# Optimization experiments

Hardware: AMD Instinct MI355X
Metric: run time of the kernel (lower is better)

## Reference

```python
import jax, jax.numpy as jnp
import numpy as np

NUM_HEADS = 16
HEAD_DIM = 64
INPUT_DIM = 1024
EMBED_DIM = NUM_HEADS * HEAD_DIM  # 1024


def setup_inputs() -> dict:
    key = jax.random.key(0)
    ks = jax.random.split(key, 9)
    B, S = 4, 2048
    scale = 1.0 / np.sqrt(INPUT_DIM)
    return {
        "q": jax.random.normal(ks[0], (B, S, INPUT_DIM), dtype=jnp.float32),
        "k": jax.random.normal(ks[1], (B, S, INPUT_DIM), dtype=jnp.float32),
        "v": jax.random.normal(ks[2], (B, S, INPUT_DIM), dtype=jnp.float32),
        "Wq": jax.random.normal(ks[3], (INPUT_DIM, EMBED_DIM), dtype=jnp.float32) * scale,
        "bq": jax.random.normal(ks[4], (EMBED_DIM,), dtype=jnp.float32) * 0.02,
        "Wk": jax.random.normal(ks[5], (INPUT_DIM, EMBED_DIM), dtype=jnp.float32) * scale,
        "bk": jax.random.normal(ks[6], (EMBED_DIM,), dtype=jnp.float32) * 0.02,
        "Wv": jax.random.normal(ks[7], (INPUT_DIM, EMBED_DIM), dtype=jnp.float32) * scale,
        "bv": jax.random.normal(ks[8], (EMBED_DIM,), dtype=jnp.float32) * 0.02,
    }


def reference(q, k, v, Wq, bq, Wk, bk, Wv, bv):
    B, Sq, _ = q.shape
    Sk = k.shape[1]
    # QKV projections (dropout_prob=0 -> identity; ReLU on value path)
    query = (q @ Wq + bq).reshape(B, Sq, NUM_HEADS, HEAD_DIM).transpose(0, 2, 1, 3)  # [B,H,Sq,D]
    key_ = (k @ Wk + bk).reshape(B, Sk, NUM_HEADS, HEAD_DIM).transpose(0, 2, 1, 3)   # [B,H,Sk,D]
    value = jax.nn.relu(v @ Wv + bv).reshape(B, Sk, NUM_HEADS, HEAD_DIM).transpose(0, 2, 1, 3)
    scores = jnp.einsum("bhqd,bhkd->bhqk", query, key_) / np.sqrt(HEAD_DIM).astype(np.float32)
    p_attn = jax.nn.softmax(scores, axis=-1)
    x = jnp.einsum("bhqk,bhkd->bhqd", p_attn, value)  # [B,H,Sq,D]
    return x.transpose(0, 2, 1, 3).reshape(B, Sq, EMBED_DIM)
```

## Files before the change

kernel.cpp:

```cpp
#include <hip/hip_runtime.h>
#include <hip/hip_bf16.h>
#include <stdint.h>

#define BB    4
#define NH    16
#define SEQ   2048
#define DH    64
#define EMB   1024
#define KD    1024
#define MROWS 8192

typedef short  short8  __attribute__((ext_vector_type(8)));
typedef float  f32x4   __attribute__((ext_vector_type(4)));
typedef float  f32x16  __attribute__((ext_vector_type(16)));

typedef const __attribute__((address_space(1))) void* gas_t;
typedef __attribute__((address_space(3))) void*       las_t;
#define GLD16(g, l) __builtin_amdgcn_global_load_lds((gas_t)(g), (las_t)(l), 16, 0, 0)

__device__ __forceinline__ unsigned short f2bf(float f) {
    unsigned u = __float_as_uint(f);
    u += 0x7fffu + ((u >> 16) & 1u);
    return (unsigned short)(u >> 16);
}
__device__ __forceinline__ unsigned packbf(float lo, float hi) {
    union { __hip_bfloat162 h; unsigned u; } cv;
    cv.h = __float22bfloat162_rn(make_float2(lo, hi));
    return cv.u;
}

__global__ __launch_bounds__(256) void conv3_kernel(const float* __restrict__ qf,
                                                    const float* __restrict__ kf,
                                                    const float* __restrict__ vf,
                                                    unsigned short* __restrict__ dst) {
    const int p = blockIdx.z;
    const float* src = (p == 0) ? qf : (p == 1) ? kf : vf;
    unsigned short* d = dst + (size_t)p * ((size_t)MROWS * KD);
    const size_t i = ((size_t)blockIdx.x * 256 + threadIdx.x) * 8;
    float4 f0 = *(const float4*)(src + i);
    float4 f1 = *(const float4*)(src + i + 4);
    uint4 u;
    u.x = packbf(f0.x, f0.y); u.y = packbf(f0.z, f0.w);
    u.z = packbf(f1.x, f1.y); u.w = packbf(f1.z, f1.w);
    *(uint4*)(d + i) = u;
}

__global__ __launch_bounds__(256) void wt_kernel(const float* __restrict__ Wq,
                                                 const float* __restrict__ Wk,
                                                 const float* __restrict__ Wv,
                                                 unsigned short* __restrict__ Wt) {
    __shared__ float tsh[64 * 68];
    const int p = blockIdx.z;
    const float* W = (p == 0) ? Wq : (p == 1) ? Wk : Wv;
    unsigned short* dst = Wt + (size_t)p * (KD * EMB);
    const int k0 = blockIdx.x * 64, n0 = blockIdx.y * 64;
    const int t = threadIdx.x;
    {
        const int r = t >> 2, c4 = (t & 3) * 16;
        const float* g = W + (size_t)(k0 + r) * EMB + n0 + c4;
        float* row = &tsh[r * 68 + c4];
        *(float4*)(row + 0)  = *(const float4*)(g + 0);
        *(float4*)(row + 4)  = *(const float4*)(g + 4);
        *(float4*)(row + 8)  = *(const float4*)(g + 8);
        *(float4*)(row + 12) = *(const float4*)(g + 12);
    }
    __syncthreads();
    {
        const int j = t >> 2, kp = (t & 3) * 16;
        unsigned ub[8];
#pragma unroll
        for (int ii = 0; ii < 8; ++ii)
            ub[ii] = packbf(tsh[(kp + 2 * ii) * 68 + j], tsh[(kp + 2 * ii + 1) * 68 + j]);
        unsigned short* o = dst + (size_t)(n0 + j) * KD + k0 + kp;
        *(uint4*)(o + 0) = uint4{ub[0], ub[1], ub[2], ub[3]};
        *(uint4*)(o + 8) = uint4{ub[4], ub[5], ub[6], ub[7]};
    }
}

__global__ __launch_bounds__(256) void proj_kernel(
    const unsigned short* __restrict__ AbfBase, const unsigned short* __restrict__ WtBase,
    const float* __restrict__ bq, const float* __restrict__ bk, const float* __restrict__ bv,
    unsigned short* __restrict__ Qg, unsigned short* __restrict__ Kg,
    unsigned short* __restrict__ Vt)
{
    __shared__ __align__(16) unsigned short smem[17408];
    unsigned short* Ash = smem;
    unsigned short* Bsh = smem + 8192;

    const int p = blockIdx.z;
    const unsigned short* Abf = AbfBase + (size_t)p * ((size_t)MROWS * KD);
    const unsigned short* Wp  = WtBase  + (size_t)p * (KD * EMB);
    const float* bias = (p == 0) ? bq : (p == 1) ? bk : bv;
    unsigned short* dst = (p == 0) ? Qg : (p == 1) ? Kg : Vt;

    const int row0 = blockIdx.x * 128;
    const int col0 = blockIdx.y * 128;
    const int t = threadIdx.x, lane = t & 63, wv = t >> 6;
    const int ln15 = lane & 15, q4 = lane >> 4;
    const int wm = wv & 1, wn = wv >> 1;

    f32x4 acc[4][4];
#pragma unroll
    for (int i = 0; i < 4; ++i)
#pragma unroll
        for (int j = 0; j < 4; ++j)
#pragma unroll
            for (int r = 0; r < 4; ++r) acc[i][j][r] = 0.f;

    const int lr = lane >> 3, lc = (lane & 7) ^ lr;
    const unsigned short* gA = Abf + (size_t)(row0 + wv * 32 + lr) * KD + lc * 8;
    const unsigned short* gB = Wp  + (size_t)(col0 + wv * 32 + lr) * KD + lc * 8;
    unsigned short* lA = Ash + wv * 32 * 64;
    unsigned short* lB = Bsh + wv * 32 * 64;

    for (int k0 = 0; k0 < KD; k0 += 64) {
#pragma unroll
        for (int i = 0; i < 4; ++i) {
            GLD16(gA + (size_t)i * 8 * KD + k0, lA + i * 512);
            GLD16(gB + (size_t)i * 8 * KD + k0, lB + i * 512);
        }
        __syncthreads();
#pragma unroll
        for (int kk = 0; kk < 2; ++kk) {
            short8 af[4], bfr[4];
#pragma unroll
            for (int mi = 0; mi < 4; ++mi) {
                const int r = wm * 64 + mi * 16 + ln15;
                af[mi] = *(const short8*)&Ash[r * 64 + (((kk << 2) | q4) ^ (r & 7)) * 8];
            }
#pragma unroll
            for (int ni = 0; ni < 4; ++ni) {
                const int r = wn * 64 + ni * 16 + ln15;
                bfr[ni] = *(const short8*)&Bsh[r * 64 + (((kk << 2) | q4) ^ (r & 7)) * 8];
            }
#pragma unroll
            for (int mi = 0; mi < 4; ++mi)
#pragma unroll
                for (int ni = 0; ni < 4; ++ni)
                    acc[mi][ni] = __builtin_amdgcn_mfma_f32_16x16x32_bf16(
                        af[mi], bfr[ni], acc[mi][ni], 0, 0, 0);
        }
        __syncthreads();
    }

    float bvv[4];
#pragma unroll
    for (int ni = 0; ni < 4; ++ni) bvv[ni] = bias[col0 + wn * 64 + ni * 16 + ln15];
    const float scq = 0.18033688011112042f;

    unsigned short* Tsh = smem;
#pragma unroll
    for (int mi = 0; mi < 4; ++mi)
#pragma unroll
        for (int ni = 0; ni < 4; ++ni)
#pragma unroll
            for (int r = 0; r < 4; ++r) {
                const int mr = wm * 64 + mi * 16 + q4 * 4 + r;
                const int ec = wn * 64 + ni * 16 + ln15;
                float vv = acc[mi][ni][r] + bvv[ni];
                if (p == 0) vv *= scq;
                if (p == 2) vv = vv > 0.f ? vv : 0.f;
                Tsh[mr * 136 + ec] = f2bf(vv);
            }
    __syncthreads();

    if (p < 2) {
        const int mr = t >> 1, hsel = t & 1;
        const int m = row0 + mr, bi = m >> 11, s = m & 2047;
        const int hh = (col0 >> 6) + hsel;
        const unsigned short* src = &Tsh[mr * 136 + hsel * 64];
        unsigned short* o = dst + ((size_t)(bi * NH + hh) * SEQ + s) * DH;
#pragma unroll
        for (int c = 0; c < 8; ++c)
            *(uint4*)(o + 8 * c) = *(const uint4*)(src + 8 * c);
    } else {
        const int e = t >> 1, sh2 = t & 1;
        const int n = col0 + e, hh = n >> 6, dd = n & 63;
        const int bi = row0 >> 11, sbase = (row0 & 2047) + sh2 * 64;
        unsigned ub[32];
#pragma unroll
        for (int i = 0; i < 32; ++i)
            ub[i] = (unsigned)Tsh[(sh2 * 64 + 2 * i) * 136 + e] |
                    ((unsigned)Tsh[(sh2 * 64 + 2 * i + 1) * 136 + e] << 16);
        unsigned short* o = dst + ((size_t)(bi * NH + hh) * DH + dd) * SEQ + sbase;
#pragma unroll
        for (int c = 0; c < 8; ++c)
            *(uint4*)(o + 8 * c) = uint4{ub[4 * c], ub[4 * c + 1], ub[4 * c + 2], ub[4 * c + 3]};
    }
}

__global__ __launch_bounds__(256) void attn_kernel(
    const unsigned short* __restrict__ Qg, const unsigned short* __restrict__ Kg,
    const unsigned short* __restrict__ Vt, float* __restrict__ out)
{
    __shared__ __align__(16) unsigned char smem[34816];
    unsigned short* Ksh = (unsigned short*)smem;
    unsigned short* Vsh = (unsigned short*)smem + 64 * 72;
    float* Osh = (float*)smem;

    const int qb = blockIdx.x, hh = blockIdx.y, bb = blockIdx.z;
    const int t = threadIdx.x, lane = t & 63, wv = t >> 6;
    const int ln31 = lane & 31, h2 = lane >> 5;
    const size_t bh = (size_t)(bb * NH + hh);
    const unsigned short* Qp = Qg + bh * (SEQ * DH);
    const unsigned short* Kp = Kg + bh * (SEQ * DH);
    const unsigned short* Vp = Vt + bh * (DH * SEQ);
    const int q0 = qb * 128 + wv * 32;

    short8 qf[4];
#pragma unroll
    for (int dc = 0; dc < 4; ++dc)
        qf[dc] = *(const short8*)(Qp + (size_t)(q0 + ln31) * DH + h2 * 8 + dc * 16);

    short8 ones;
#pragma unroll
    for (int i = 0; i < 8; ++i) ones[i] = (short)0x3F80;

    f32x16 accO[2], accL;
#pragma unroll
    for (int i = 0; i < 16; ++i) { accO[0][i] = 0.f; accO[1][i] = 0.f; accL[i] = 0.f; }

    const int srow = t >> 2, sp = (t & 3) * 16;
    const unsigned short* gk = Kp + (size_t)srow * DH + sp;
    const unsigned short* gv = Vp + (size_t)srow * SEQ + sp;
    unsigned short* lk = &Ksh[srow * 72 + sp];
    unsigned short* lv = &Vsh[srow * 72 + sp];

    for (int kt0 = 0; kt0 < SEQ; kt0 += 64) {
        __syncthreads();
        *(short8*)lk       = *(const short8*)(gk + (size_t)kt0 * DH);
        *(short8*)(lk + 8) = *(const short8*)(gk + (size_t)kt0 * DH + 8);
        *(short8*)lv       = *(const short8*)(gv + kt0);
        *(short8*)(lv + 8) = *(const short8*)(gv + kt0 + 8);
        __syncthreads();

        f32x16 st[2];
#pragma unroll
        for (int kt = 0; kt < 2; ++kt) {
#pragma unroll
            for (int i = 0; i < 16; ++i) st[kt][i] = 0.f;
#pragma unroll
            for (int dc = 0; dc < 4; ++dc) {
                short8 kf = *(const short8*)&Ksh[(kt * 32 + ln31) * 72 + h2 * 8 + dc * 16];
                st[kt] = __builtin_amdgcn_mfma_f32_32x32x16_bf16(kf, qf[dc], st[kt], 0, 0, 0);
            }
        }
#pragma unroll
        for (int kt = 0; kt < 2; ++kt)
#pragma unroll
            for (int r = 0; r < 16; ++r)
                st[kt][r] = __builtin_amdgcn_exp2f(st[kt][r]);

#pragma unroll
        for (int kt = 0; kt < 2; ++kt) {
            unsigned ow[8], xw[8];
#pragma unroll
            for (int i = 0; i < 8; ++i) {
                ow[i] = packbf(st[kt][2 * i], st[kt][2 * i + 1]);
                xw[i] = (unsigned)__shfl_xor((int)ow[i], 32);
            }
#pragma unroll
            for (int kc = 0; kc < 2; ++kc) {
                union { unsigned u[4]; short8 v; } pf;
                pf.u[0] = h2 ? xw[4 * kc + 2] : ow[4 * kc + 0];
                pf.u[1] = h2 ? xw[4 * kc + 3] : ow[4 * kc + 1];
                pf.u[2] = h2 ? ow[4 * kc + 2] : xw[4 * kc + 0];
                pf.u[3] = h2 ? ow[4 * kc + 3] : xw[4 * kc + 1];
                const int nc = kt * 2 + kc;
                accL = __builtin_amdgcn_mfma_f32_32x32x16_bf16(ones, pf.v, accL, 0, 0, 0);
#pragma unroll
                for (int dt = 0; dt < 2; ++dt) {
                    short8 vf = *(const short8*)&Vsh[(dt * 32 + ln31) * 72 + nc * 16 + h2 * 8];
                    accO[dt] = __builtin_amdgcn_mfma_f32_32x32x16_bf16(vf, pf.v, accO[dt], 0, 0, 0);
                }
            }
        }
    }

    const float inv = 1.0f / accL[0];
    __syncthreads();
#pragma unroll
    for (int dt = 0; dt < 2; ++dt)
#pragma unroll
        for (int r = 0; r < 16; ++r) {
            const int d = dt * 32 + (r & 3) + 8 * (r >> 2) + 4 * h2;
            Osh[(wv * 32 + ln31) * 68 + d] = accO[dt][r] * inv;
        }
    __syncthreads();
    const int r128 = t >> 1, dh = t & 1;
    float* op = out + (((size_t)(bb * SEQ + qb * 128 + r128) * NH + hh) << 6) + dh * 32;
    const float* osrc = &Osh[r128 * 68 + dh * 32];
#pragma unroll
    for (int c = 0; c < 8; ++c)
        *(float4*)(op + 4 * c) = *(const float4*)(osrc + 4 * c);
}

extern "C" void kernel_launch(void* const* d_in, const int* in_sizes, int n_in,
                              void* d_out, int out_size, void* d_ws, size_t ws_size,
                              hipStream_t stream) {
    const float* qf = (const float*)d_in[0];
    const float* kf = (const float*)d_in[1];
    const float* vf = (const float*)d_in[2];
    const float* Wq = (const float*)d_in[3];
    const float* bq = (const float*)d_in[4];
    const float* Wk = (const float*)d_in[5];
    const float* bk = (const float*)d_in[6];
    const float* Wv = (const float*)d_in[7];
    const float* bv = (const float*)d_in[8];

    char* ws = (char*)d_ws;
    unsigned short* Wt  = (unsigned short*)ws;
    unsigned short* Qg  = (unsigned short*)(ws + 6291456);
    unsigned short* Kg  = Qg + 8388608;
    unsigned short* Vt  = Kg + 8388608;
    unsigned short* Ab  = Vt + 8388608;
    float* out = (float*)d_out;

    wt_kernel<<<dim3(16, 16, 3), 256, 0, stream>>>(Wq, Wk, Wv, Wt);
    conv3_kernel<<<dim3(4096, 1, 3), 256, 0, stream>>>(qf, kf, vf, Ab);
    proj_kernel<<<dim3(64, 8, 3), 256, 0, stream>>>(Ab, Wt, bq, bk, bv, Qg, Kg, Vt);
    attn_kernel<<<dim3(16, 16, 4), 256, 0, stream>>>(Qg, Kg, Vt, out);
}
```

Measured before the change: 350.9 us.

## Enlarge projection GEMM tile to 256 rows and store attention output directly

The projection GEMM now computes 256x128 tiles per block, with each wave holding an 8x4 accumulator grid. This halves the grid and cuts weight reloads per output row, at the cost of more registers, more LDS, and a two-pass epilogue through shared memory. The attention kernel drops its LDS staging of the output and writes float4 fragments straight from registers to global memory. That shrinks its shared memory and removes two barriers, but the global writes become less contiguous.

```diff
diff --git a/kernel.cpp b/kernel.cpp
--- a/kernel.cpp
+++ b/kernel.cpp
@@ -83,9 +83,9 @@
     unsigned short* __restrict__ Qg, unsigned short* __restrict__ Kg,
     unsigned short* __restrict__ Vt)
 {
-    __shared__ __align__(16) unsigned short smem[17408];
+    __shared__ __align__(16) unsigned short smem[24576];
     unsigned short* Ash = smem;
-    unsigned short* Bsh = smem + 8192;
+    unsigned short* Bsh = smem + 16384;
 
     const int p = blockIdx.z;
     const unsigned short* Abf = AbfBase + (size_t)p * ((size_t)MROWS * KD);
@@ -93,48 +93,50 @@
     const float* bias = (p == 0) ? bq : (p == 1) ? bk : bv;
     unsigned short* dst = (p == 0) ? Qg : (p == 1) ? Kg : Vt;
 
-    const int row0 = blockIdx.x * 128;
+    const int row0 = blockIdx.x * 256;
     const int col0 = blockIdx.y * 128;
     const int t = threadIdx.x, lane = t & 63, wv = t >> 6;
     const int ln15 = lane & 15, q4 = lane >> 4;
     const int wm = wv & 1, wn = wv >> 1;
 
-    f32x4 acc[4][4];
-#pragma unroll
-    for (int i = 0; i < 4; ++i)
+    f32x4 acc[8][4];
+#pragma unroll
+    for (int i = 0; i < 8; ++i)
 #pragma unroll
         for (int j = 0; j < 4; ++j)
 #pragma unroll
             for (int r = 0; r < 4; ++r) acc[i][j][r] = 0.f;
 
     const int lr = lane >> 3, lc = (lane & 7) ^ lr;
-    const unsigned short* gA = Abf + (size_t)(row0 + wv * 32 + lr) * KD + lc * 8;
+    const unsigned short* gA = Abf + (size_t)(row0 + wv * 64 + lr) * KD + lc * 8;
     const unsigned short* gB = Wp  + (size_t)(col0 + wv * 32 + lr) * KD + lc * 8;
-    unsigned short* lA = Ash + wv * 32 * 64;
+    unsigned short* lA = Ash + wv * 64 * 64;
     unsigned short* lB = Bsh + wv * 32 * 64;
 
     for (int k0 = 0; k0 < KD; k0 += 64) {
 #pragma unroll
-        for (int i = 0; i < 4; ++i) {
+        for (int i = 0; i < 8; ++i)
             GLD16(gA + (size_t)i * 8 * KD + k0, lA + i * 512);
+#pragma unroll
+        for (int i = 0; i < 4; ++i)
             GLD16(gB + (size_t)i * 8 * KD + k0, lB + i * 512);
-        }
         __syncthreads();
 #pragma unroll
         for (int kk = 0; kk < 2; ++kk) {
-            short8 af[4], bfr[4];
-#pragma unroll
-            for (int mi = 0; mi < 4; ++mi) {
-                const int r = wm * 64 + mi * 16 + ln15;
-                af[mi] = *(const short8*)&Ash[r * 64 + (((kk << 2) | q4) ^ (r & 7)) * 8];
-            }
+            const int ck = (kk << 2) | q4;
+            short8 af[8], bfr[4];
 #pragma unroll
             for (int ni = 0; ni < 4; ++ni) {
                 const int r = wn * 64 + ni * 16 + ln15;
-                bfr[ni] = *(const short8*)&Bsh[r * 64 + (((kk << 2) | q4) ^ (r & 7)) * 8];
-            }
-#pragma unroll
-            for (int mi = 0; mi < 4; ++mi)
+                bfr[ni] = *(const short8*)&Bsh[r * 64 + (ck ^ (r & 7)) * 8];
+            }
+#pragma unroll
+            for (int mi = 0; mi < 8; ++mi) {
+                const int r = wm * 128 + mi * 16 + ln15;
+                af[mi] = *(const short8*)&Ash[r * 64 + (ck ^ (r & 7)) * 8];
+            }
+#pragma unroll
+            for (int mi = 0; mi < 8; ++mi)
 #pragma unroll
                 for (int ni = 0; ni < 4; ++ni)
                     acc[mi][ni] = __builtin_amdgcn_mfma_f32_16x16x32_bf16(
@@ -150,42 +152,48 @@
 
     unsigned short* Tsh = smem;
 #pragma unroll
-    for (int mi = 0; mi < 4; ++mi)
-#pragma unroll
-        for (int ni = 0; ni < 4; ++ni)
-#pragma unroll
-            for (int r = 0; r < 4; ++r) {
-                const int mr = wm * 64 + mi * 16 + q4 * 4 + r;
-                const int ec = wn * 64 + ni * 16 + ln15;
-                float vv = acc[mi][ni][r] + bvv[ni];
-                if (p == 0) vv *= scq;
-                if (p == 2) vv = vv > 0.f ? vv : 0.f;
-                Tsh[mr * 136 + ec] = f2bf(vv);
-            }
-    __syncthreads();
-
-    if (p < 2) {
-        const int mr = t >> 1, hsel = t & 1;
-        const int m = row0 + mr, bi = m >> 11, s = m & 2047;
-        const int hh = (col0 >> 6) + hsel;
-        const unsigned short* src = &Tsh[mr * 136 + hsel * 64];
-        unsigned short* o = dst + ((size_t)(bi * NH + hh) * SEQ + s) * DH;
-#pragma unroll
-        for (int c = 0; c < 8; ++c)
-            *(uint4*)(o + 8 * c) = *(const uint4*)(src + 8 * c);
-    } else {
-        const int e = t >> 1, sh2 = t & 1;
-        const int n = col0 + e, hh = n >> 6, dd = n & 63;
-        const int bi = row0 >> 11, sbase = (row0 & 2047) + sh2 * 64;
-        unsigned ub[32];
-#pragma unroll
-        for (int i = 0; i < 32; ++i)
-            ub[i] = (unsigned)Tsh[(sh2 * 64 + 2 * i) * 136 + e] |
-                    ((unsigned)Tsh[(sh2 * 64 + 2 * i + 1) * 136 + e] << 16);
-        unsigned short* o = dst + ((size_t)(bi * NH + hh) * DH + dd) * SEQ + sbase;
-#pragma unroll
-        for (int c = 0; c < 8; ++c)
-            *(uint4*)(o + 8 * c) = uint4{ub[4 * c], ub[4 * c + 1], ub[4 * c + 2], ub[4 * c + 3]};
+    for (int h = 0; h < 2; ++h) {
+        if (wm == h) {
+#pragma unroll
+            for (int mi = 0; mi < 8; ++mi)
+#pragma unroll
+                for (int ni = 0; ni < 4; ++ni)
+#pragma unroll
+                    for (int r = 0; r < 4; ++r) {
+                        const int mr = mi * 16 + q4 * 4 + r;
+                        const int ec = wn * 64 + ni * 16 + ln15;
+                        float vv = acc[mi][ni][r] + bvv[ni];
+                        if (p == 0) vv *= scq;
+                        if (p == 2) vv = vv > 0.f ? vv : 0.f;
+                        Tsh[mr * 136 + ec] = f2bf(vv);
+                    }
+        }
+        __syncthreads();
+        if (p < 2) {
+            const int mr = t >> 1, hsel = t & 1;
+            const int m = row0 + h * 128 + mr, bi = m >> 11, s = m & 2047;
+            const int hh = (col0 >> 6) + hsel;
+            const unsigned short* src = &Tsh[mr * 136 + hsel * 64];
+            unsigned short* o = dst + ((size_t)(bi * NH + hh) * SEQ + s) * DH;
+#pragma unroll
+            for (int c = 0; c < 8; ++c)
+                *(uint4*)(o + 8 * c) = *(const uint4*)(src + 8 * c);
+        } else {
+            const int e = t >> 1, sh2 = t & 1;
+            const int n = col0 + e, hh = n >> 6, dd = n & 63;
+            const int bi = row0 >> 11;
+            const int sbase = (row0 & 2047) + h * 128 + sh2 * 64;
+            unsigned ub[32];
+#pragma unroll
+            for (int i = 0; i < 32; ++i)
+                ub[i] = (unsigned)Tsh[(sh2 * 64 + 2 * i) * 136 + e] |
+                        ((unsigned)Tsh[(sh2 * 64 + 2 * i + 1) * 136 + e] << 16);
+            unsigned short* o = dst + ((size_t)(bi * NH + hh) * DH + dd) * SEQ + sbase;
+#pragma unroll
+            for (int c = 0; c < 8; ++c)
+                *(uint4*)(o + 8 * c) = uint4{ub[4 * c], ub[4 * c + 1], ub[4 * c + 2], ub[4 * c + 3]};
+        }
+        __syncthreads();
     }
 }
 
@@ -193,10 +201,9 @@
     const unsigned short* __restrict__ Qg, const unsigned short* __restrict__ Kg,
     const unsigned short* __restrict__ Vt, float* __restrict__ out)
 {
-    __shared__ __align__(16) unsigned char smem[34816];
+    __shared__ __align__(16) unsigned char smem[18432];
     unsigned short* Ksh = (unsigned short*)smem;
     unsigned short* Vsh = (unsigned short*)smem + 64 * 72;
-    float* Osh = (float*)smem;
 
     const int qb = blockIdx.x, hh = blockIdx.y, bb = blockIdx.z;
     const int t = threadIdx.x, lane = t & 63, wv = t >> 6;
@@ -278,21 +285,18 @@
     }
 
     const float inv = 1.0f / accL[0];
-    __syncthreads();
+    float* orow = out + ((size_t)(bb * SEQ + q0 + ln31) * NH + hh) * 64;
 #pragma unroll
     for (int dt = 0; dt < 2; ++dt)
 #pragma unroll
-        for (int r = 0; r < 16; ++r) {
-            const int d = dt * 32 + (r & 3) + 8 * (r >> 2) + 4 * h2;
-            Osh[(wv * 32 + ln31) * 68 + d] = accO[dt][r] * inv;
-        }
-    __syncthreads();
-    const int r128 = t >> 1, dh = t & 1;
-    float* op = out + (((size_t)(bb * SEQ + qb * 128 + r128) * NH + hh) << 6) + dh * 32;
-    const float* osrc = &Osh[r128 * 68 + dh * 32];
-#pragma unroll
-    for (int c = 0; c < 8; ++c)
-        *(float4*)(op + 4 * c) = *(const float4*)(osrc + 4 * c);
+        for (int g = 0; g < 4; ++g) {
+            float4 w;
+            w.x = accO[dt][4 * g + 0] * inv;
+            w.y = accO[dt][4 * g + 1] * inv;
+            w.z = accO[dt][4 * g + 2] * inv;
+            w.w = accO[dt][4 * g + 3] * inv;
+            *(float4*)(orow + dt * 32 + 4 * h2 + 8 * g) = w;
+        }
 }
 
 extern "C" void kernel_launch(void* const* d_in, const int* in_sizes, int n_in,
@@ -318,6 +322,6 @@
 
     wt_kernel<<<dim3(16, 16, 3), 256, 0, stream>>>(Wq, Wk, Wv, Wt);
     conv3_kernel<<<dim3(4096, 1, 3), 256, 0, stream>>>(qf, kf, vf, Ab);
-    proj_kernel<<<dim3(64, 8, 3), 256, 0, stream>>>(Ab, Wt, bq, bk, bv, Qg, Kg, Vt);
+    proj_kernel<<<dim3(32, 8, 3), 256, 0, stream>>>(Ab, Wt, bq, bk, bv, Qg, Kg, Vt);
     attn_kernel<<<dim3(16, 16, 4), 256, 0, stream>>>(Qg, Kg, Vt, out);
 }
```

Result: slower. 386.5 us (+10.2%).

## Load K/V MFMA fragments directly from global memory, drop LDS staging

Applied to the files above, without the earlier changes.

The attention kernel no longer stages K and V tiles in shared memory with barriers. Each wave now loads its MFMA operand fragments straight from global memory into registers, and the output is written directly from accumulators without an LDS transpose. This removes the two barriers per tile and the LDS traffic. In exchange, each of the four waves re-reads the same K/V tile from global/L2, which quadruples that traffic, and the loads become less coalesced and raise register pressure.

```diff
diff --git a/kernel.cpp b/kernel.cpp
--- a/kernel.cpp
+++ b/kernel.cpp
@@ -193,18 +193,13 @@
     const unsigned short* __restrict__ Qg, const unsigned short* __restrict__ Kg,
     const unsigned short* __restrict__ Vt, float* __restrict__ out)
 {
-    __shared__ __align__(16) unsigned char smem[34816];
-    unsigned short* Ksh = (unsigned short*)smem;
-    unsigned short* Vsh = (unsigned short*)smem + 64 * 72;
-    float* Osh = (float*)smem;
-
     const int qb = blockIdx.x, hh = blockIdx.y, bb = blockIdx.z;
     const int t = threadIdx.x, lane = t & 63, wv = t >> 6;
     const int ln31 = lane & 31, h2 = lane >> 5;
     const size_t bh = (size_t)(bb * NH + hh);
     const unsigned short* Qp = Qg + bh * (SEQ * DH);
-    const unsigned short* Kp = Kg + bh * (SEQ * DH);
-    const unsigned short* Vp = Vt + bh * (DH * SEQ);
+    const unsigned short* Kp = Kg + bh * (SEQ * DH) + (size_t)ln31 * DH  + h2 * 8;
+    const unsigned short* Vp = Vt + bh * (DH * SEQ) + (size_t)ln31 * SEQ + h2 * 8;
     const int q0 = qb * 128 + wv * 32;
 
     short8 qf[4];
@@ -220,19 +215,20 @@
 #pragma unroll
     for (int i = 0; i < 16; ++i) { accO[0][i] = 0.f; accO[1][i] = 0.f; accL[i] = 0.f; }
 
-    const int srow = t >> 2, sp = (t & 3) * 16;
-    const unsigned short* gk = Kp + (size_t)srow * DH + sp;
-    const unsigned short* gv = Vp + (size_t)srow * SEQ + sp;
-    unsigned short* lk = &Ksh[srow * 72 + sp];
-    unsigned short* lv = &Vsh[srow * 72 + sp];
-
     for (int kt0 = 0; kt0 < SEQ; kt0 += 64) {
-        __syncthreads();
-        *(short8*)lk       = *(const short8*)(gk + (size_t)kt0 * DH);
-        *(short8*)(lk + 8) = *(const short8*)(gk + (size_t)kt0 * DH + 8);
-        *(short8*)lv       = *(const short8*)(gv + kt0);
-        *(short8*)(lv + 8) = *(const short8*)(gv + kt0 + 8);
-        __syncthreads();
+        short8 kfr[2][4];
+#pragma unroll
+        for (int kt = 0; kt < 2; ++kt)
+#pragma unroll
+            for (int dc = 0; dc < 4; ++dc)
+                kfr[kt][dc] = *(const short8*)(Kp + (size_t)(kt0 + kt * 32) * DH + dc * 16);
+
+        short8 vfr[2][4];
+#pragma unroll
+        for (int dt = 0; dt < 2; ++dt)
+#pragma unroll
+            for (int nc = 0; nc < 4; ++nc)
+                vfr[dt][nc] = *(const short8*)(Vp + (size_t)(dt * 32) * SEQ + kt0 + nc * 16);
 
         f32x16 st[2];
 #pragma unroll
@@ -240,10 +236,8 @@
 #pragma unroll
             for (int i = 0; i < 16; ++i) st[kt][i] = 0.f;
 #pragma unroll
-            for (int dc = 0; dc < 4; ++dc) {
-                short8 kf = *(const short8*)&Ksh[(kt * 32 + ln31) * 72 + h2 * 8 + dc * 16];
-                st[kt] = __builtin_amdgcn_mfma_f32_32x32x16_bf16(kf, qf[dc], st[kt], 0, 0, 0);
-            }
+            for (int dc = 0; dc < 4; ++dc)
+                st[kt] = __builtin_amdgcn_mfma_f32_32x32x16_bf16(kfr[kt][dc], qf[dc], st[kt], 0, 0, 0);
         }
 #pragma unroll
         for (int kt = 0; kt < 2; ++kt)
@@ -269,30 +263,25 @@
                 const int nc = kt * 2 + kc;
                 accL = __builtin_amdgcn_mfma_f32_32x32x16_bf16(ones, pf.v, accL, 0, 0, 0);
 #pragma unroll
-                for (int dt = 0; dt < 2; ++dt) {
-                    short8 vf = *(const short8*)&Vsh[(dt * 32 + ln31) * 72 + nc * 16 + h2 * 8];
-                    accO[dt] = __builtin_amdgcn_mfma_f32_32x32x16_bf16(vf, pf.v, accO[dt], 0, 0, 0);
-                }
+                for (int dt = 0; dt < 2; ++dt)
+                    accO[dt] = __builtin_amdgcn_mfma_f32_32x32x16_bf16(vfr[dt][nc], pf.v, accO[dt], 0, 0, 0);
             }
         }
     }
 
     const float inv = 1.0f / accL[0];
-    __syncthreads();
+    float* orow = out + ((size_t)(bb * SEQ + q0 + ln31) * NH + hh) * 64;
 #pragma unroll
     for (int dt = 0; dt < 2; ++dt)
 #pragma unroll
-        for (int r = 0; r < 16; ++r) {
-            const int d = dt * 32 + (r & 3) + 8 * (r >> 2) + 4 * h2;
-            Osh[(wv * 32 + ln31) * 68 + d] = accO[dt][r] * inv;
-        }
-    __syncthreads();
-    const int r128 = t >> 1, dh = t & 1;
-    float* op = out + (((size_t)(bb * SEQ + qb * 128 + r128) * NH + hh) << 6) + dh * 32;
-    const float* osrc = &Osh[r128 * 68 + dh * 32];
-#pragma unroll
-    for (int c = 0; c < 8; ++c)
-        *(float4*)(op + 4 * c) = *(const float4*)(osrc + 4 * c);
+        for (int g = 0; g < 4; ++g) {
+            float4 w;
+            w.x = accO[dt][4 * g + 0] * inv;
+            w.y = accO[dt][4 * g + 1] * inv;
+            w.z = accO[dt][4 * g + 2] * inv;
+            w.w = accO[dt][4 * g + 3] * inv;
+            *(float4*)(orow + dt * 32 + 4 * h2 + 8 * g) = w;
+        }
 }
 
 extern "C" void kernel_launch(void* const* d_in, const int* in_sizes, int n_in,
```

Measured after the change: 468.0 us. 1.33x slower.
